# Kernel optimization log

Hardware: AMD Instinct MI355X
Metric: run time of the kernel (lower is better)

The kernel has to match this reference:

```python
import jax, jax.numpy as jnp
import numpy as np

D = 1024
S = 2048
B = 4


def setup_inputs() -> dict:
    key = jax.random.key(0)
    ks = jax.random.split(key, 9)
    sc = 1.0 / np.sqrt(D)
    return {
        "x": jax.random.normal(ks[0], (B, S, D), dtype=jnp.float32),
        "Wq": jax.random.normal(ks[1], (D, D), dtype=jnp.float32) * sc,
        "bq": jax.random.normal(ks[2], (D,), dtype=jnp.float32) * 0.02,
        "Wk": jax.random.normal(ks[3], (D, D), dtype=jnp.float32) * sc,
        "bk": jax.random.normal(ks[4], (D,), dtype=jnp.float32) * 0.02,
        "Wv": jax.random.normal(ks[5], (D, D), dtype=jnp.float32) * sc,
        "bv": jax.random.normal(ks[6], (D,), dtype=jnp.float32) * 0.02,
        "Wp": jax.random.normal(ks[7], (D, D), dtype=jnp.float32) * sc,
        "bp": jax.random.normal(ks[8], (D,), dtype=jnp.float32) * 0.02,
    }


def reference(x, Wq, bq, Wk, bk, Wv, bv, Wp, bp):
    # torch nn.Linear: y = x @ W.T + b  (W stored [out, in])
    q = jnp.einsum("bsd,ed->bse", x, Wq) + bq  # [B,S,D]
    k = jnp.einsum("bsd,ed->bse", x, Wk) + bk
    v = jnp.einsum("bsd,ed->bse", x, Wv) + bv

    scale = 1.0 / jnp.sqrt(jnp.asarray(q.shape[-1], q.dtype))
    # single-head attention: contract over full embd_dim (no head split in source)
    scores = jnp.einsum("bqd,bkd->bqk", q, k) * scale  # [B,S,S]

    seq = x.shape[1]
    causal = jnp.tril(jnp.ones((seq, seq), dtype=bool))  # [S,S]
    scores = jnp.where(causal[None, :, :], scores, -jnp.inf)

    attn = jax.nn.softmax(scores, axis=-1)  # [B,S,S]
    out = jnp.einsum("bqk,bkd->bqd", attn, v)  # [B,S,D]
    out = jnp.einsum("bsd,ed->bse", out, Wp) + bp
    return out
```

## Files before the change

### kernel.cpp

```cpp
#include <hip/hip_runtime.h>

#define AS1(p) ((const __attribute__((address_space(1))) void*)(p))
#define AS3(p) ((__attribute__((address_space(3))) void*)(p))

typedef unsigned short u16;
typedef __bf16 bf16x8 __attribute__((ext_vector_type(8)));
typedef short s16x8 __attribute__((ext_vector_type(8)));
typedef float f32x4 __attribute__((ext_vector_type(4)));
typedef unsigned short u16x4 __attribute__((ext_vector_type(4)));
typedef unsigned short u16x8v __attribute__((ext_vector_type(8)));

__device__ __forceinline__ u16 f2bf(float x) {
    unsigned u = __float_as_uint(x);
    unsigned r = (u + 0x7FFFu + ((u >> 16) & 1u)) >> 16;
    return (u16)r;
}

template <typename V8>
__device__ __forceinline__ auto mfma_sel(V8 a, V8 b, f32x4 c, int)
    -> decltype(__builtin_amdgcn_mfma_f32_16x16x32_bf16(a, b, c, 0, 0, 0))
{
    return __builtin_amdgcn_mfma_f32_16x16x32_bf16(a, b, c, 0, 0, 0);
}
template <typename V8>
__device__ __forceinline__ f32x4 mfma_sel(V8 a, V8 b, f32x4 c, long)
{
    s16x8 a2 = __builtin_bit_cast(s16x8, a);
    s16x8 b2 = __builtin_bit_cast(s16x8, b);
    return __builtin_amdgcn_mfma_f32_16x16x32_bf16(a2, b2, c, 0, 0, 0);
}
__device__ __forceinline__ f32x4 mfma16x16x32(bf16x8 a, bf16x8 b, f32x4 c)
{
    return mfma_sel(a, b, c, 0);
}

__global__ __launch_bounds__(256) void cvt_all_kernel(const float* __restrict__ x,
                                                      const float* __restrict__ Wq,
                                                      const float* __restrict__ Wk,
                                                      const float* __restrict__ Wv,
                                                      const float* __restrict__ Wp,
                                                      u16* __restrict__ xb,
                                                      u16* __restrict__ Wcat,
                                                      u16* __restrict__ Wpb,
                                                      float* __restrict__ rsum,
                                                      int n4x, int n4w, int nrs)
{
    int i = blockIdx.x * 256 + threadIdx.x;
    const int total = n4x + 4 * n4w;
    if (i >= total) {
        int j = i - total;
        if (j < nrs) rsum[j] = 0.f;
        return;
    }
    const float* src;
    u16* dst;
    int off;
    if (i < n4x) {
        src = x; dst = xb; off = i;
    } else {
        int j = i - n4x;
        int w = j >> 18;
        off = j & (n4w - 1);
        src = (w == 0) ? Wq : (w == 1) ? Wk : (w == 2) ? Wv : Wp;
        dst = (w == 3) ? Wpb : (Wcat + (size_t)w * n4w * 4);
    }
    float4 f = ((const float4*)src)[off];
    u16x4 o;
    o.x = f2bf(f.x); o.y = f2bf(f.y); o.z = f2bf(f.z); o.w = f2bf(f.w);
    ((u16x4*)dst)[off] = o;
}

__global__ __launch_bounds__(256) void transpose16(const u16* __restrict__ in,
                                                   u16* __restrict__ out, int R, int C)
{
    __shared__ u16 tl[64][65];
    const int tr0 = blockIdx.y * 64, tc0 = blockIdx.x * 64;
    const int t = threadIdx.x;
    const int r = t >> 2, c4 = (t & 3) << 4;

    const u16* src = in + (size_t)(tr0 + r) * C + tc0 + c4;
    u16x8v a0 = *(const u16x8v*)src;
    u16x8v a1 = *(const u16x8v*)(src + 8);
    #pragma unroll
    for (int j = 0; j < 8; ++j) { tl[r][c4 + j] = a0[j]; tl[r][c4 + 8 + j] = a1[j]; }
    __syncthreads();

    u16x8v b0, b1;
    #pragma unroll
    for (int j = 0; j < 8; ++j) { b0[j] = tl[c4 + j][r]; b1[j] = tl[c4 + 8 + j][r]; }
    u16* dst = out + (size_t)(tc0 + r) * R + tr0 + c4;
    *(u16x8v*)dst = b0;
    *(u16x8v*)(dst + 8) = b1;
}

#define MBM 128
#define MBK 64

template <int BIAS, int OUTBF16, int CSKIP, int CKB, int SWZ, int MW, int EXPOUT, int RDIV>
__global__ __launch_bounds__(256, MW)
void gemm128(const u16* __restrict__ A, const u16* __restrict__ B,
             void* __restrict__ Cv, const float* __restrict__ bias,
             void* __restrict__ C2, const float* __restrict__ bias2,
             void* __restrict__ C3, const float* __restrict__ bias3,
             float* __restrict__ rsum,
             int M, int N, int K, int lda, int ldb, int ldc,
             long long sA, long long sB, long long sC, float scale)
{
    __shared__ u16 lA[MBM * MBK];
    __shared__ u16 lB[MBM * MBK];

    int bx = blockIdx.x, by = blockIdx.y;
    if (SWZ) {
        const int gx = gridDim.x;
        const int nwg = gx * gridDim.y;
        int id = by * gx + bx;
        id = (id & 7) * (nwg >> 3) + (id >> 3);
        bx = id % gx; by = id / gx;
    }
    if (CKB) by = gridDim.y - 1 - by;
    const int m0 = by * MBM;
    const int n0 = bx * MBM;
    if (CSKIP && n0 > m0 + MBM - 1) return;

    const int z = blockIdx.z;
    A += (size_t)z * (size_t)sA;
    B += (size_t)z * (size_t)sB;

    const int t = threadIdx.x;
    const int lane = t & 63;
    const int w = t >> 6;
    const int wr = w >> 1;
    const int wc = w & 1;
    const int fr = lane & 15, fg = lane >> 4;

    int Keff = K;
    if (CKB) { Keff = m0 + MBM; if (Keff > K) Keff = K; }
    const int nk = Keff / MBK;

    f32x4 acc[4][4] = {};

    for (int kt = 0; kt < nk; ++kt) {
        const int k0 = kt * MBK;
        #pragma unroll
        for (int i = 0; i < 4; ++i) {
            int c = t + i * 256;
            int row = c >> 3;
            int sl = (c & 7) ^ (row & 7);
            __builtin_amdgcn_global_load_lds(
                AS1(A + (size_t)(m0 + row) * lda + k0 + sl * 8),
                AS3(&lA[c * 8]), 16, 0, 0);
            __builtin_amdgcn_global_load_lds(
                AS1(B + (size_t)(n0 + row) * ldb + k0 + sl * 8),
                AS3(&lB[c * 8]), 16, 0, 0);
        }
        __syncthreads();

        #pragma unroll
        for (int kk = 0; kk < MBK; kk += 32) {
            const int cs = (kk >> 3) + fg;
            bf16x8 af[4], bfv[4];
            #pragma unroll
            for (int mi = 0; mi < 4; ++mi) {
                int row = wr * 64 + mi * 16 + fr;
                af[mi] = *(const bf16x8*)&lA[row * 64 + ((cs ^ (row & 7)) << 3)];
            }
            #pragma unroll
            for (int ni = 0; ni < 4; ++ni) {
                int row = wc * 64 + ni * 16 + fr;
                bfv[ni] = *(const bf16x8*)&lB[row * 64 + ((cs ^ (row & 7)) << 3)];
            }
            __builtin_amdgcn_s_setprio(1);
            #pragma unroll
            for (int mi = 0; mi < 4; ++mi)
                #pragma unroll
                for (int ni = 0; ni < 4; ++ni)
                    acc[mi][ni] = mfma16x16x32(af[mi], bfv[ni], acc[mi][ni]);
            __builtin_amdgcn_s_setprio(0);
        }
        __syncthreads();
    }

    if (EXPOUT) {
        float prs[4][4];
        #pragma unroll
        for (int mi = 0; mi < 4; ++mi)
            #pragma unroll
            for (int j = 0; j < 4; ++j) prs[mi][j] = 0.f;
        #pragma unroll
        for (int mi = 0; mi < 4; ++mi) {
            int row0 = m0 + wr * 64 + mi * 16 + fg * 4;
            #pragma unroll
            for (int ni = 0; ni < 4; ++ni) {
                int col = n0 + wc * 64 + ni * 16 + fr;
                #pragma unroll
                for (int j = 0; j < 4; ++j) {
                    int row = row0 + j;
                    float p = (col <= row) ? __expf(acc[mi][ni][j] - 16.f) : 0.f;
                    ((u16*)Cv)[(size_t)z * (size_t)sC + (size_t)row * ldc + col] = f2bf(p);
                    prs[mi][j] += p;
                }
            }
        }
        #pragma unroll
        for (int mi = 0; mi < 4; ++mi) {
            #pragma unroll
            for (int j = 0; j < 4; ++j) {
                float s = prs[mi][j];
                s += __shfl_xor(s, 1); s += __shfl_xor(s, 2);
                s += __shfl_xor(s, 4); s += __shfl_xor(s, 8);
                if (fr == 0)
                    atomicAdd(&rsum[(size_t)z * M + m0 + wr * 64 + mi * 16 + fg * 4 + j], s);
            }
        }
        return;
    }

    #pragma unroll
    for (int mi = 0; mi < 4; ++mi) {
        int row0 = m0 + wr * 64 + mi * 16 + fg * 4;
        float invr[4];
        if (RDIV) {
            #pragma unroll
            for (int j = 0; j < 4; ++j)
                invr[j] = 1.f / rsum[(size_t)z * M + row0 + j];
        }
        #pragma unroll
        for (int ni = 0; ni < 4; ++ni) {
            int col = n0 + wc * 64 + ni * 16 + fr;
            if (BIAS == 3) {
                int seg = col >> 10;
                int ccol = col & 1023;
                u16* dst = (seg == 0) ? (u16*)Cv : (seg == 1) ? (u16*)C2 : (u16*)C3;
                float b = ((seg == 0) ? bias : (seg == 1) ? bias2 : bias3)[ccol];
                float sc_ = (seg == 0) ? scale : 1.f;
                #pragma unroll
                for (int j = 0; j < 4; ++j)
                    dst[(size_t)(row0 + j) * 1024 + ccol] =
                        f2bf((acc[mi][ni][j] + b) * sc_);
            } else {
                float bval = (BIAS == 1) ? bias[col] : 0.f;
                #pragma unroll
                for (int j = 0; j < 4; ++j) {
                    float v = RDIV ? acc[mi][ni][j] * invr[j]
                                   : (acc[mi][ni][j] + bval) * scale;
                    size_t off = (size_t)z * (size_t)sC + (size_t)(row0 + j) * ldc + col;
                    if (OUTBF16) ((u16*)Cv)[off] = f2bf(v);
                    else         ((float*)Cv)[off] = v;
                }
            }
        }
    }
}

extern "C" void kernel_launch(void* const* d_in, const int* in_sizes, int n_in,
                              void* d_out, int out_size, void* d_ws, size_t ws_size,
                              hipStream_t stream)
{
    (void)in_sizes; (void)n_in; (void)out_size; (void)ws_size;
    const float* x  = (const float*)d_in[0];
    const float* Wq = (const float*)d_in[1];
    const float* bq = (const float*)d_in[2];
    const float* Wk = (const float*)d_in[3];
    const float* bk = (const float*)d_in[4];
    const float* Wv = (const float*)d_in[5];
    const float* bv = (const float*)d_in[6];
    const float* Wp = (const float*)d_in[7];
    const float* bp = (const float*)d_in[8];

    const int D = 1024, S = 2048, B = 4;
    const int M = B * S;

    char* p = (char*)d_ws;
    u16* xb    = (u16*)p; p += (size_t)M * D * 2;
    u16* Wpb   = (u16*)p; p += (size_t)D * D * 2;
    u16* qb    = (u16*)p; p += (size_t)M * D * 2;
    u16* kb    = (u16*)p; p += (size_t)M * D * 2;
    float* rsum = (float*)p; p += (size_t)B * S * 4;
    u16* Wcat  = (u16*)p;
    u16* vb    = (u16*)(p + (size_t)3 * D * D * 2);
    u16* sc    = (u16*)p;
    u16* vTb   = xb;
    u16* attnb = kb;

    const int n4x = M * D / 4;
    const int n4w = D * D / 4;
    const int nrs = B * S;

    cvt_all_kernel<<<(n4x + 4 * n4w + nrs + 255) / 256, 256, 0, stream>>>(
        x, Wq, Wk, Wv, Wp, xb, Wcat, Wpb, rsum, n4x, n4w, nrs);

    gemm128<3, 1, 0, 0, 1, 3, 0, 0><<<dim3(3 * D / MBM, M / MBM), 256, 0, stream>>>(
        xb, Wcat, qb, bq, kb, bk, vb, bv, nullptr,
        M, 3 * D, D, D, D, D, 0, 0, 0, 0.03125f);

    transpose16<<<dim3(D / 64, M / 64), 256, 0, stream>>>(vb, vTb, M, D);

    gemm128<0, 1, 1, 0, 0, 4, 1, 0><<<dim3(S / MBM, S / MBM, B), 256, 0, stream>>>(
        qb, kb, sc, nullptr, nullptr, nullptr, nullptr, nullptr, rsum,
        S, S, D, D, D, S,
        (long long)S * D, (long long)S * D, (long long)S * S, 1.0f);

    gemm128<0, 1, 0, 1, 0, 4, 0, 1><<<dim3(D / MBM, S / MBM, B), 256, 0, stream>>>(
        sc, vTb, attnb, nullptr, nullptr, nullptr, nullptr, nullptr, rsum,
        S, D, S, S, M, D,
        (long long)S * S, (long long)S, (long long)S * D, 1.0f);

    gemm128<1, 0, 0, 0, 1, 4, 0, 0><<<dim3(D / MBM, M / MBM), 256, 0, stream>>>(
        attnb, Wpb, d_out, bp, nullptr, nullptr, nullptr, nullptr, nullptr,
        M, D, D, D, D, D, 0, 0, 0, 1.0f);
}
```

Before: 185.4 us.

## Fuse V transpose into QK^T launch and pack causal score matrix

Removes the standalone transpose launch by adding an extra z-slice to the QK^T grid whose blocks each transpose eight 64x64 tiles of V. The score matrix is stored in a packed lower-triangular row-block layout, where each 128-row block has row stride (blk+1)*128. This cuts score memory and the bytes written and read for the masked upper triangle. The PV GEMM reads A through the same packed addressing. The risk is that the transpose blocks become stragglers alongside the causal-skip blocks, and the workspace layout changes.

Result: faster. 180.4 us (-2.7%).

```diff
diff --git a/kernel.cpp b/kernel.cpp
--- a/kernel.cpp
+++ b/kernel.cpp
@@ -70,33 +70,11 @@
     ((u16x4*)dst)[off] = o;
 }
 
-__global__ __launch_bounds__(256) void transpose16(const u16* __restrict__ in,
-                                                   u16* __restrict__ out, int R, int C)
-{
-    __shared__ u16 tl[64][65];
-    const int tr0 = blockIdx.y * 64, tc0 = blockIdx.x * 64;
-    const int t = threadIdx.x;
-    const int r = t >> 2, c4 = (t & 3) << 4;
-
-    const u16* src = in + (size_t)(tr0 + r) * C + tc0 + c4;
-    u16x8v a0 = *(const u16x8v*)src;
-    u16x8v a1 = *(const u16x8v*)(src + 8);
-    #pragma unroll
-    for (int j = 0; j < 8; ++j) { tl[r][c4 + j] = a0[j]; tl[r][c4 + 8 + j] = a1[j]; }
-    __syncthreads();
-
-    u16x8v b0, b1;
-    #pragma unroll
-    for (int j = 0; j < 8; ++j) { b0[j] = tl[c4 + j][r]; b1[j] = tl[c4 + 8 + j][r]; }
-    u16* dst = out + (size_t)(tc0 + r) * R + tr0 + c4;
-    *(u16x8v*)dst = b0;
-    *(u16x8v*)(dst + 8) = b1;
-}
-
 #define MBM 128
 #define MBK 64
 
-template <int BIAS, int OUTBF16, int CSKIP, int CKB, int SWZ, int MW, int EXPOUT, int RDIV>
+template <int BIAS, int OUTBF16, int CSKIP, int CKB, int SWZ, int MW,
+          int EXPOUT, int RDIV, int PACKA, int FUSET>
 __global__ __launch_bounds__(256, MW)
 void gemm128(const u16* __restrict__ A, const u16* __restrict__ B,
              void* __restrict__ Cv, const float* __restrict__ bias,
@@ -109,6 +87,40 @@
     __shared__ u16 lA[MBM * MBK];
     __shared__ u16 lB[MBM * MBK];
 
+    if (FUSET && blockIdx.z == 4) {
+        const u16* vin = (const u16*)C2;
+        u16* vout = (u16*)C3;
+        u16* tl = lA;
+        const int t = threadIdx.x;
+        const int r = t >> 2, c4 = (t & 3) << 4;
+        const int bid = blockIdx.y * 16 + blockIdx.x;
+        for (int it = 0; it < 8; ++it) {
+            const int tile = bid * 8 + it;
+            const int tc0 = (tile & 15) * 64;
+            const int tr0 = (tile >> 4) * 64;
+            const u16* src = vin + (size_t)(tr0 + r) * 1024 + tc0 + c4;
+            u16x8v a0 = *(const u16x8v*)src;
+            u16x8v a1 = *(const u16x8v*)(src + 8);
+            #pragma unroll
+            for (int j = 0; j < 8; ++j) {
+                tl[r * 65 + c4 + j] = a0[j];
+                tl[r * 65 + c4 + 8 + j] = a1[j];
+            }
+            __syncthreads();
+            u16x8v b0, b1;
+            #pragma unroll
+            for (int j = 0; j < 8; ++j) {
+                b0[j] = tl[(c4 + j) * 65 + r];
+                b1[j] = tl[(c4 + 8 + j) * 65 + r];
+            }
+            u16* dst = vout + (size_t)(tc0 + r) * 8192 + tr0 + c4;
+            *(u16x8v*)dst = b0;
+            *(u16x8v*)(dst + 8) = b1;
+            __syncthreads();
+        }
+        return;
+    }
+
     int bx = blockIdx.x, by = blockIdx.y;
     if (SWZ) {
         const int gx = gridDim.x;
@@ -123,7 +135,14 @@
     if (CSKIP && n0 > m0 + MBM - 1) return;
 
     const int z = blockIdx.z;
-    A += (size_t)z * (size_t)sA;
+    const int ablk = m0 >> 7;
+    long long abase = (long long)z * sA;
+    int lda_e = lda;
+    if (PACKA) {
+        lda_e = (ablk + 1) << 7;
+        abase -= (long long)8192 * ablk * (ablk + 1);
+    }
+    const u16* Ab = A + abase;
     B += (size_t)z * (size_t)sB;
 
     const int t = threadIdx.x;
@@ -147,7 +166,7 @@
             int row = c >> 3;
             int sl = (c & 7) ^ (row & 7);
             __builtin_amdgcn_global_load_lds(
-                AS1(A + (size_t)(m0 + row) * lda + k0 + sl * 8),
+                AS1(Ab + (long long)(m0 + row) * lda_e + k0 + sl * 8),
                 AS3(&lA[c * 8]), 16, 0, 0);
             __builtin_amdgcn_global_load_lds(
                 AS1(B + (size_t)(n0 + row) * ldb + k0 + sl * 8),
@@ -181,6 +200,8 @@
     }
 
     if (EXPOUT) {
+        const int ldcp = (ablk + 1) << 7;
+        u16* Cp = (u16*)Cv + ((long long)z * sC - (long long)8192 * ablk * (ablk + 1));
         float prs[4][4];
         #pragma unroll
         for (int mi = 0; mi < 4; ++mi)
@@ -196,7 +217,7 @@
                 for (int j = 0; j < 4; ++j) {
                     int row = row0 + j;
                     float p = (col <= row) ? __expf(acc[mi][ni][j] - 16.f) : 0.f;
-                    ((u16*)Cv)[(size_t)z * (size_t)sC + (size_t)row * ldc + col] = f2bf(p);
+                    Cp[(long long)row * ldcp + col] = f2bf(p);
                     prs[mi][j] += p;
                 }
             }
@@ -269,6 +290,7 @@
 
     const int D = 1024, S = 2048, B = 4;
     const int M = B * S;
+    const long long sP = 16384LL * 136;
 
     char* p = (char*)d_ws;
     u16* xb    = (u16*)p; p += (size_t)M * D * 2;
@@ -276,9 +298,9 @@
     u16* qb    = (u16*)p; p += (size_t)M * D * 2;
     u16* kb    = (u16*)p; p += (size_t)M * D * 2;
     float* rsum = (float*)p; p += (size_t)B * S * 4;
-    u16* Wcat  = (u16*)p;
-    u16* vb    = (u16*)(p + (size_t)3 * D * D * 2);
-    u16* sc    = (u16*)p;
+    u16* vb    = (u16*)p; p += (size_t)M * D * 2;
+    u16* scp   = (u16*)p;
+    u16* Wcat  = scp;
     u16* vTb   = xb;
     u16* attnb = kb;
 
@@ -289,23 +311,21 @@
     cvt_all_kernel<<<(n4x + 4 * n4w + nrs + 255) / 256, 256, 0, stream>>>(
         x, Wq, Wk, Wv, Wp, xb, Wcat, Wpb, rsum, n4x, n4w, nrs);
 
-    gemm128<3, 1, 0, 0, 1, 3, 0, 0><<<dim3(3 * D / MBM, M / MBM), 256, 0, stream>>>(
+    gemm128<3, 1, 0, 0, 1, 3, 0, 0, 0, 0><<<dim3(3 * D / MBM, M / MBM), 256, 0, stream>>>(
         xb, Wcat, qb, bq, kb, bk, vb, bv, nullptr,
         M, 3 * D, D, D, D, D, 0, 0, 0, 0.03125f);
 
-    transpose16<<<dim3(D / 64, M / 64), 256, 0, stream>>>(vb, vTb, M, D);
-
-    gemm128<0, 1, 1, 0, 0, 4, 1, 0><<<dim3(S / MBM, S / MBM, B), 256, 0, stream>>>(
-        qb, kb, sc, nullptr, nullptr, nullptr, nullptr, nullptr, rsum,
-        S, S, D, D, D, S,
-        (long long)S * D, (long long)S * D, (long long)S * S, 1.0f);
-
-    gemm128<0, 1, 0, 1, 0, 4, 0, 1><<<dim3(D / MBM, S / MBM, B), 256, 0, stream>>>(
-        sc, vTb, attnb, nullptr, nullptr, nullptr, nullptr, nullptr, rsum,
-        S, D, S, S, M, D,
-        (long long)S * S, (long long)S, (long long)S * D, 1.0f);
-
-    gemm128<1, 0, 0, 0, 1, 4, 0, 0><<<dim3(D / MBM, M / MBM), 256, 0, stream>>>(
+    gemm128<0, 1, 1, 0, 0, 4, 1, 0, 0, 1><<<dim3(S / MBM, S / MBM, B + 1), 256, 0, stream>>>(
+        qb, kb, scp, nullptr, vb, nullptr, vTb, nullptr, rsum,
+        S, S, D, D, D, 0,
+        (long long)S * D, (long long)S * D, sP, 1.0f);
+
+    gemm128<0, 1, 0, 1, 0, 4, 0, 1, 1, 0><<<dim3(D / MBM, S / MBM, B), 256, 0, stream>>>(
+        scp, vTb, attnb, nullptr, nullptr, nullptr, nullptr, nullptr, rsum,
+        S, D, S, 0, M, D,
+        sP, (long long)S, (long long)S * D, 1.0f);
+
+    gemm128<1, 0, 0, 0, 1, 4, 0, 0, 0, 0><<<dim3(D / MBM, M / MBM), 256, 0, stream>>>(
         attnb, Wpb, d_out, bp, nullptr, nullptr, nullptr, nullptr, nullptr,
         M, D, D, D, D, D, 0, 0, 0, 1.0f);
 }
```
